# Kernel optimization log

Measured on AMD Instinct MI355X. Metric: run time of the kernel, lower is better.

The kernel has to match this reference:

```python
import jax, jax.numpy as jnp
import numpy as np

NEG_SLOPE = 0.2  # PyG GATConv default negative_slope


def gat_conv(x, edge_index, W, att_src, att_dst, bias):
    """PyG-style GATConv (concat heads, add_self_loops=True, eval mode).
    x: [N, F_in], edge_index: [2, E] (row 0 = src j, row 1 = dst i).
    W: [F_in, H*C], att_src/att_dst: [H, C], bias: [H*C].
    """
    N = x.shape[0]
    H, C = att_src.shape
    loops = jnp.arange(N, dtype=edge_index.dtype)
    src = jnp.concatenate([edge_index[0], loops])  # [E+N]
    dst = jnp.concatenate([edge_index[1], loops])
    h = (x @ W).reshape(N, H, C)                              # [N,H,C]
    a_src = jnp.einsum('nhc,hc->nh', h, att_src)              # [N,H]
    a_dst = jnp.einsum('nhc,hc->nh', h, att_dst)
    alpha = jax.nn.leaky_relu(a_src[src] + a_dst[dst], NEG_SLOPE)  # [E+N,H]
    # segment softmax over edges sharing the same destination node
    m = jax.ops.segment_max(alpha, dst, num_segments=N)       # [N,H]
    e = jnp.exp(alpha - jax.lax.stop_gradient(m)[dst])
    denom = jax.ops.segment_sum(e, dst, num_segments=N)       # [N,H]
    a = e / (denom[dst] + 1e-16)                              # [E+N,H]
    msg = h[src] * a[:, :, None]                              # [E+N,H,C]
    out = jax.ops.segment_sum(msg, dst, num_segments=N)       # [N,H,C]
    return out.reshape(N, H * C) + bias


def setup_inputs() -> dict:
    key = jax.random.key(0)
    ks = jax.random.split(key, 10)
    N, F, NC, C1, H1 = 50000, 128, 40, 16, 8
    E = 800000
    x = jax.random.normal(ks[0], (N, F), dtype=jnp.float32)
    edge_index = jax.random.randint(ks[1], (2, E), 0, N, dtype=jnp.int64)
    s1 = 1.0 / np.sqrt(F)
    W1 = jax.random.uniform(ks[2], (F, H1 * C1), jnp.float32, -s1, s1)
    att_src1 = jax.random.uniform(ks[3], (H1, C1), jnp.float32, -1.0, 1.0) * s1
    att_dst1 = jax.random.uniform(ks[4], (H1, C1), jnp.float32, -1.0, 1.0) * s1
    bias1 = jnp.zeros((H1 * C1,), jnp.float32)
    s2 = 1.0 / np.sqrt(H1 * C1)
    W2 = jax.random.uniform(ks[5], (H1 * C1, NC), jnp.float32, -s2, s2)
    att_src2 = jax.random.uniform(ks[6], (1, NC), jnp.float32, -1.0, 1.0) * s2
    att_dst2 = jax.random.uniform(ks[7], (1, NC), jnp.float32, -1.0, 1.0) * s2
    bias2 = jnp.zeros((NC,), jnp.float32)
    return {"x": x, "edge_index": edge_index, "W1": W1, "att_src1": att_src1,
            "att_dst1": att_dst1, "bias1": bias1, "W2": W2, "att_src2": att_src2,
            "att_dst2": att_dst2, "bias2": bias2}


def reference(x, edge_index, W1, att_src1, att_dst1, bias1, W2, att_src2, att_dst2, bias2):
    h = gat_conv(x, edge_index, W1, att_src1, att_dst1, bias1)   # [N, 128]
    # dropout in eval mode = identity
    out = gat_conv(h, edge_index, W2, att_src2, att_dst2, bias2)  # [N, 40]
    return out
```

## Files before the change

### kernel.cpp

```cpp
#include <hip/hip_runtime.h>
#include <hip/hip_bf16.h>
#include <math.h>

#define NEG_SLOPE 0.2f

typedef __bf16 bf16x8 __attribute__((ext_vector_type(8)));
typedef float f32x4 __attribute__((ext_vector_type(4)));

__device__ __forceinline__ float lrelu(float x) { return x > 0.f ? x : NEG_SLOPE * x; }

__device__ __forceinline__ unsigned short f2bfu(float f) {
    unsigned int ua = __float_as_uint(f);
    return (unsigned short)((ua + 0x7fffu + ((ua >> 16) & 1u)) >> 16);
}
__device__ __forceinline__ float bfu2f(unsigned short u) {
    return __uint_as_float(((unsigned int)u) << 16);
}
__device__ __forceinline__ float bf_lo(unsigned int u) { return __uint_as_float(u << 16); }
__device__ __forceinline__ float bf_hi(unsigned int u) { return __uint_as_float(u & 0xffff0000u); }

__global__ __launch_bounds__(256) void k_prep(const float* __restrict__ W1,
                                              bf16x8* __restrict__ Wp,
                                              const float* __restrict__ W2,
                                              bf16x8* __restrict__ W2p,
                                              int* __restrict__ cnt, int N) {
    int g = blockIdx.x * 256 + threadIdx.x;
    if (g < 2048) {
        int n = g & 15, quad = (g >> 4) & 3, c = (g >> 6) & 3, ct = g >> 8;
        bf16x8 v;
#pragma unroll
        for (int j = 0; j < 8; ++j)
            v[j] = (__bf16)W1[(c * 32 + quad * 8 + j) * 128 + ct * 16 + n];
        Wp[g] = v;
    } else if (g < 2816) {
        int idx = g - 2048;
        int n = idx & 15, quad = (idx >> 4) & 3, c = (idx >> 6) & 3, ct = idx >> 8;
        int colc = ct * 16 + n;
        bf16x8 v;
#pragma unroll
        for (int j = 0; j < 8; ++j)
            v[j] = (colc < 40) ? (__bf16)W2[(c * 32 + quad * 8 + j) * 40 + colc] : (__bf16)0.f;
        W2p[idx] = v;
    }
    if (g < N) cnt[g] = 0;
}

__global__ __launch_bounds__(256) void k_hist(const int* __restrict__ ei, int E, int N,
                                              int* __restrict__ cnt,
                                              unsigned short* __restrict__ rank) {
    int e = blockIdx.x * 256 + threadIdx.x;
    if (e >= E + N) return;
    int d = (e < E) ? ei[E + e] : (e - E);
    rank[e] = (unsigned short)atomicAdd(&cnt[d], 1);
}

__global__ __launch_bounds__(256) void k_scan_part(const int* __restrict__ cnt, int N,
                                                   int* __restrict__ psum) {
    __shared__ int sh[256];
    int t = threadIdx.x;
    int base = blockIdx.x * 1024 + t * 4;
    int tl = 0;
#pragma unroll
    for (int j = 0; j < 4; ++j) tl += (base + j < N) ? cnt[base + j] : 0;
    sh[t] = tl; __syncthreads();
    for (int off = 128; off > 0; off >>= 1) {
        if (t < off) sh[t] += sh[t + off];
        __syncthreads();
    }
    if (t == 0) psum[blockIdx.x] = sh[0];
}

__global__ __launch_bounds__(256) void k_scan_add(const int* __restrict__ cnt, int N,
                                                  const int* __restrict__ psum,
                                                  int* __restrict__ rowptr) {
    __shared__ int sh[256];
    __shared__ int basep;
    int t = threadIdx.x;
    if (t == 0) {
        int s = 0;
        for (int i = 0; i < blockIdx.x; ++i) s += psum[i];
        basep = s;
    }
    int base = blockIdx.x * 1024 + t * 4;
    int c[4]; int tl = 0;
#pragma unroll
    for (int j = 0; j < 4; ++j) { c[j] = (base + j < N) ? cnt[base + j] : 0; tl += c[j]; }
    sh[t] = tl; __syncthreads();
    for (int off = 1; off < 256; off <<= 1) {
        int a = (t >= off) ? sh[t - off] : 0;
        __syncthreads();
        sh[t] += a;
        __syncthreads();
    }
    int run = basep + (sh[t] - tl);
#pragma unroll
    for (int j = 0; j < 4; ++j) {
        if (base + j < N) { rowptr[base + j] = run; run += c[j]; }
    }
}

__global__ __launch_bounds__(256) void k_scatter(const int* __restrict__ ei, int E, int N,
                                                 const int* __restrict__ rowptr,
                                                 const unsigned short* __restrict__ rank,
                                                 unsigned short* __restrict__ col) {
    int e = blockIdx.x * 256 + threadIdx.x;
    if (e >= E + N) return;
    int s, d;
    if (e < E) { s = ei[e]; d = ei[E + e]; } else { s = d = e - E; }
    col[rowptr[d] + (int)rank[e]] = (unsigned short)s;
}

__global__ __launch_bounds__(256) void k_gemm1(const float* __restrict__ x,
                                               const bf16x8* __restrict__ Wp,
                                               const float* __restrict__ att_s,
                                               const float* __restrict__ att_d,
                                               unsigned short* __restrict__ h1A,
                                               unsigned short* __restrict__ h1B,
                                               float* __restrict__ a_src,
                                               float* __restrict__ a_dst, int N) {
    int t = threadIdx.x;
    int w = t >> 6, lane = t & 63, quad = lane >> 4, n16 = lane & 15;
    int row0 = blockIdx.x * 64 + w * 16;
    int arow = row0 + n16; if (arow >= N) arow = N - 1;
    const float* px = x + (size_t)arow * 128;

    bf16x8 ah[4], al[4];
#pragma unroll
    for (int c = 0; c < 4; ++c) {
        float4 v0 = *(const float4*)&px[c * 32 + quad * 8];
        float4 v1 = *(const float4*)&px[c * 32 + quad * 8 + 4];
        float xf[8] = {v0.x, v0.y, v0.z, v0.w, v1.x, v1.y, v1.z, v1.w};
#pragma unroll
        for (int j = 0; j < 8; ++j) {
            __bf16 hi = (__bf16)xf[j];
            ah[c][j] = hi;
            al[c][j] = (__bf16)(xf[j] - (float)hi);
        }
    }

    f32x4 acc[8];
#pragma unroll
    for (int ct = 0; ct < 8; ++ct) acc[ct] = (f32x4){0.f, 0.f, 0.f, 0.f};

    const uint4* wp4 = (const uint4*)Wp;
#pragma unroll
    for (int ct = 0; ct < 8; ++ct) {
#pragma unroll
        for (int c = 0; c < 4; ++c) {
            union { uint4 u; bf16x8 b; } bu;
            bu.u = wp4[((ct * 4 + c) * 4 + quad) * 16 + n16];
            acc[ct] = __builtin_amdgcn_mfma_f32_16x16x32_bf16(ah[c], bu.b, acc[ct], 0, 0, 0);
            acc[ct] = __builtin_amdgcn_mfma_f32_16x16x32_bf16(al[c], bu.b, acc[ct], 0, 0, 0);
        }
    }

    float asv[8], adv[8];
#pragma unroll
    for (int ct = 0; ct < 8; ++ct) {
        asv[ct] = att_s[ct * 16 + n16];
        adv[ct] = att_d[ct * 16 + n16];
    }
    int nodeb = row0 + quad * 4;
#pragma unroll
    for (int ct = 0; ct < 8; ++ct) {
        unsigned short* hp = (ct < 4) ? h1A : h1B;
        int chl = (ct & 3) * 16 + n16;
#pragma unroll
        for (int reg = 0; reg < 4; ++reg) {
            int node = nodeb + reg;
            float hv = acc[ct][reg];
            float ps = hv * asv[ct];
            float pd = hv * adv[ct];
#pragma unroll
            for (int m = 1; m < 16; m <<= 1) {
                ps += __shfl_xor(ps, m);
                pd += __shfl_xor(pd, m);
            }
            if (node < N) {
                hp[(size_t)node * 64 + chl] = f2bfu(hv);
                if (n16 == 0) {
                    a_src[(size_t)node * 8 + ct] = ps;
                    a_dst[(size_t)node * 8 + ct] = pd;
                }
            }
        }
    }
}

__global__ __launch_bounds__(256) void k_aggr1(const int* __restrict__ rowptr,
                                               const int* __restrict__ cnt,
                                               const unsigned short* __restrict__ col,
                                               const float* __restrict__ a_src,
                                               const float* __restrict__ a_dst,
                                               const unsigned int* __restrict__ h1A,
                                               const unsigned int* __restrict__ h1B,
                                               const float* __restrict__ bias1,
                                               unsigned int* __restrict__ out1h,
                                               unsigned int* __restrict__ out1l,
                                               int N, int nag) {
    __shared__ float evs[4][2][128];
    __shared__ int   cls[4][2][32];
    int p = (blockIdx.x >= nag) ? 1 : 0;
    int blk = blockIdx.x - p * nag;
    const uint4* hp4 = (const uint4*)(p ? h1B : h1A);
    int t = threadIdx.x;
    int w = t >> 6;
    int lane = t & 63;
    int half = lane >> 5;
    int u = lane & 31;
    int e4 = u >> 3;
    int v  = u & 7;
    int hh = v >> 1;
    int node = blk * 8 + w * 2 + half;
    bool nv = (node < N);
    int nodec = nv ? node : (N - 1);
    int beg = rowptr[nodec];
    int deg = nv ? cnt[nodec] : 0;
    int degO = __shfl_xor(deg, 32);
    int degmax = (deg > degO) ? deg : degO;
    if (degmax <= 0) return;

    float4 ad4 = *(const float4*)&a_dst[(size_t)nodec * 8 + p * 4];
    float* myev = &evs[w][half][0];
    int*   mycl = &cls[w][half][0];

    float den = 0.f;
    float nm[8];
#pragma unroll
    for (int k = 0; k < 8; ++k) nm[k] = 0.f;

    int c = 0;
    while (c < degmax) {
        int slot = c + u;
        int slotc = (slot < deg) ? slot : (deg - 1);
        if (slotc < 0) slotc = 0;
        int su = (int)col[beg + slotc];
        float4 as4 = *(const float4*)&a_src[(size_t)su * 8 + p * 4];
        bool valid = (slot < deg);
        float e0 = valid ? __expf(lrelu(as4.x + ad4.x)) : 0.f;
        float e1 = valid ? __expf(lrelu(as4.y + ad4.y)) : 0.f;
        float e2 = valid ? __expf(lrelu(as4.z + ad4.z)) : 0.f;
        float e3 = valid ? __expf(lrelu(as4.w + ad4.w)) : 0.f;
        *(float4*)&myev[u * 4] = make_float4(e0, e1, e2, e3);
        mycl[u] = su;

        int ccm = degmax - c; ccm = (ccm < 32) ? ccm : 32;
        int ng = (ccm + 3) >> 2;
        int gl = ng - 1;
        int g1 = (1 < gl) ? 1 : gl;
        int g2 = (2 < gl) ? 2 : gl;
        int g3 = (3 < gl) ? 3 : gl;
        uint4 U0 = hp4[mycl[e4] * 8 + v];
        uint4 U1 = hp4[mycl[g1 * 4 + e4] * 8 + v];
        uint4 U2 = hp4[mycl[g2 * 4 + e4] * 8 + v];
        uint4 U3 = hp4[mycl[g3 * 4 + e4] * 8 + v];
        int body = ng - 4;
        int g = 0;
#pragma unroll 2
        for (; g < body; ++g) {
            uint4 UN = hp4[mycl[(g + 4) * 4 + e4] * 8 + v];
            float ev = myev[(g * 4 + e4) * 4 + hh];
            den += ev;
            nm[0] = fmaf(ev, bf_lo(U0.x), nm[0]);
            nm[1] = fmaf(ev, bf_hi(U0.x), nm[1]);
            nm[2] = fmaf(ev, bf_lo(U0.y), nm[2]);
            nm[3] = fmaf(ev, bf_hi(U0.y), nm[3]);
            nm[4] = fmaf(ev, bf_lo(U0.z), nm[4]);
            nm[5] = fmaf(ev, bf_hi(U0.z), nm[5]);
            nm[6] = fmaf(ev, bf_lo(U0.w), nm[6]);
            nm[7] = fmaf(ev, bf_hi(U0.w), nm[7]);
            U0 = U1; U1 = U2; U2 = U3; U3 = UN;
        }
        for (; g < ng; ++g) {
            float ev = myev[(g * 4 + e4) * 4 + hh];
            den += ev;
            nm[0] = fmaf(ev, bf_lo(U0.x), nm[0]);
            nm[1] = fmaf(ev, bf_hi(U0.x), nm[1]);
            nm[2] = fmaf(ev, bf_lo(U0.y), nm[2]);
            nm[3] = fmaf(ev, bf_hi(U0.y), nm[3]);
            nm[4] = fmaf(ev, bf_lo(U0.z), nm[4]);
            nm[5] = fmaf(ev, bf_hi(U0.z), nm[5]);
            nm[6] = fmaf(ev, bf_lo(U0.w), nm[6]);
            nm[7] = fmaf(ev, bf_hi(U0.w), nm[7]);
            U0 = U1; U1 = U2; U2 = U3;
        }
        c += 32;
    }
    den += __shfl_xor(den, 8);
    den += __shfl_xor(den, 16);
#pragma unroll
    for (int k = 0; k < 8; ++k) {
        nm[k] += __shfl_xor(nm[k], 8);
        nm[k] += __shfl_xor(nm[k], 16);
    }
    if (nv && e4 == 0) {
        float inv = 1.f / (den + 1e-16f);
        float4 b0 = *(const float4*)&bias1[p * 64 + v * 8];
        float4 b1 = *(const float4*)&bias1[p * 64 + v * 8 + 4];
        float bb[8] = {b0.x, b0.y, b0.z, b0.w, b1.x, b1.y, b1.z, b1.w};
        unsigned int H[4], L[4];
#pragma unroll
        for (int q = 0; q < 4; ++q) {
            float o0 = fmaf(nm[2 * q],     inv, bb[2 * q]);
            float o1 = fmaf(nm[2 * q + 1], inv, bb[2 * q + 1]);
            unsigned short h0 = f2bfu(o0), h1 = f2bfu(o1);
            float l0 = o0 - bfu2f(h0), l1 = o1 - bfu2f(h1);
            H[q] = (unsigned int)h0 | ((unsigned int)h1 << 16);
            L[q] = (unsigned int)f2bfu(l0) | ((unsigned int)f2bfu(l1) << 16);
        }
        size_t idx = (size_t)node * 64 + p * 32 + v * 4;
        *(uint4*)&out1h[idx] = make_uint4(H[0], H[1], H[2], H[3]);
        *(uint4*)&out1l[idx] = make_uint4(L[0], L[1], L[2], L[3]);
    }
}

__global__ __launch_bounds__(256) void k_gemm2(const unsigned int* __restrict__ out1h,
                                               const unsigned int* __restrict__ out1l,
                                               const bf16x8* __restrict__ W2p,
                                               const float* __restrict__ att_s2,
                                               const float* __restrict__ att_d2,
                                               unsigned short* __restrict__ h2s,
                                               float* __restrict__ a_src2,
                                               float* __restrict__ a_dst2, int N) {
    int t = threadIdx.x;
    int w = t >> 6, lane = t & 63, quad = lane >> 4, n16 = lane & 15;
    int row0 = blockIdx.x * 64 + w * 16;
    int arow = row0 + n16; if (arow >= N) arow = N - 1;

    bf16x8 ah[4], al[4];
#pragma unroll
    for (int c = 0; c < 4; ++c) {
        size_t base = (size_t)arow * 64 + (c * 32 + quad * 8) / 2;
        union { uint4 u; bf16x8 b; } hu, lu;
        hu.u = *(const uint4*)&out1h[base];
        lu.u = *(const uint4*)&out1l[base];
        ah[c] = hu.b;
        al[c] = lu.b;
    }

    f32x4 acc[3];
#pragma unroll
    for (int ct = 0; ct < 3; ++ct) acc[ct] = (f32x4){0.f, 0.f, 0.f, 0.f};

    const uint4* wp4 = (const uint4*)W2p;
#pragma unroll
    for (int ct = 0; ct < 3; ++ct) {
#pragma unroll
        for (int c = 0; c < 4; ++c) {
            union { uint4 u; bf16x8 b; } bu;
            bu.u = wp4[((ct * 4 + c) * 4 + quad) * 16 + n16];
            acc[ct] = __builtin_amdgcn_mfma_f32_16x16x32_bf16(ah[c], bu.b, acc[ct], 0, 0, 0);
            acc[ct] = __builtin_amdgcn_mfma_f32_16x16x32_bf16(al[c], bu.b, acc[ct], 0, 0, 0);
        }
    }

    float asv[3], adv[3];
#pragma unroll
    for (int ct = 0; ct < 3; ++ct) {
        int ch = ct * 16 + n16;
        asv[ct] = (ch < 40) ? att_s2[ch] : 0.f;
        adv[ct] = (ch < 40) ? att_d2[ch] : 0.f;
    }
    int nodeb = row0 + quad * 4;
#pragma unroll
    for (int reg = 0; reg < 4; ++reg) {
        int node = nodeb + reg;
        float ps = 0.f, pd = 0.f;
#pragma unroll
        for (int ct = 0; ct < 3; ++ct) {
            float hv = acc[ct][reg];
            ps = fmaf(hv, asv[ct], ps);
            pd = fmaf(hv, adv[ct], pd);
            int ch = ct * 16 + n16;
            if (node < N && ch < 40) h2s[(size_t)node * 64 + ch] = f2bfu(hv);
        }
#pragma unroll
        for (int m = 1; m < 16; m <<= 1) {
            ps += __shfl_xor(ps, m);
            pd += __shfl_xor(pd, m);
        }
        if (node < N && n16 == 0) {
            a_src2[node] = ps;
            a_dst2[node] = pd;
        }
    }
}

__global__ __launch_bounds__(256) void k_aggr2(const int* __restrict__ rowptr,
                                               const int* __restrict__ cnt,
                                               const unsigned short* __restrict__ col,
                                               const float* __restrict__ a_src,
                                               const float* __restrict__ a_dst,
                                               const unsigned int* __restrict__ h2b,
                                               const float* __restrict__ bias2,
                                               float* __restrict__ out, int N) {
    __shared__ float evs[4][2][32];
    __shared__ int   cls[4][2][32];
    int t = threadIdx.x;
    int w = t >> 6;
    int lane = t & 63;
    int half = lane >> 5;
    int u = lane & 31;
    int e4 = u >> 3;
    int v  = u & 7;
    int node = blockIdx.x * 8 + w * 2 + half;
    bool nv = (node < N);
    int nodec = nv ? node : (N - 1);
    int beg = rowptr[nodec];
    int deg = nv ? cnt[nodec] : 0;
    int degO = __shfl_xor(deg, 32);
    int degmax = (deg > degO) ? deg : degO;
    if (degmax <= 0) return;

    const uint4* h24 = (const uint4*)h2b;
    float ad = a_dst[nodec];
    float* myev = &evs[w][half][0];
    int*   mycl = &cls[w][half][0];

    float den = 0.f;
    float am[8];
#pragma unroll
    for (int k = 0; k < 8; ++k) am[k] = 0.f;

    int c = 0;
    while (c < degmax) {
        int slot = c + u;
        int slotc = (slot < deg) ? slot : (deg - 1);
        if (slotc < 0) slotc = 0;
        int su = (int)col[beg + slotc];
        float ev = (slot < deg) ? __expf(lrelu(a_src[su] + ad)) : 0.f;
        myev[u] = ev;
        mycl[u] = su;

        int ccm = degmax - c; ccm = (ccm < 32) ? ccm : 32;
        int ng = (ccm + 3) >> 2;
        int gl = ng - 1;
        int g1 = (1 < gl) ? 1 : gl;
        int g2 = (2 < gl) ? 2 : gl;
        int g3 = (3 < gl) ? 3 : gl;
        uint4 U0 = h24[mycl[e4] * 8 + v];
        uint4 U1 = h24[mycl[g1 * 4 + e4] * 8 + v];
        uint4 U2 = h24[mycl[g2 * 4 + e4] * 8 + v];
        uint4 U3 = h24[mycl[g3 * 4 + e4] * 8 + v];
        int body = ng - 4;
        int g = 0;
#pragma unroll 2
        for (; g < body; ++g) {
            uint4 UN = h24[mycl[(g + 4) * 4 + e4] * 8 + v];
            float evv = myev[g * 4 + e4];
            den += evv;
            am[0] = fmaf(evv, bf_lo(U0.x), am[0]);
            am[1] = fmaf(evv, bf_hi(U0.x), am[1]);
            am[2] = fmaf(evv, bf_lo(U0.y), am[2]);
            am[3] = fmaf(evv, bf_hi(U0.y), am[3]);
            am[4] = fmaf(evv, bf_lo(U0.z), am[4]);
            am[5] = fmaf(evv, bf_hi(U0.z), am[5]);
            am[6] = fmaf(evv, bf_lo(U0.w), am[6]);
            am[7] = fmaf(evv, bf_hi(U0.w), am[7]);
            U0 = U1; U1 = U2; U2 = U3; U3 = UN;
        }
        for (; g < ng; ++g) {
            float evv = myev[g * 4 + e4];
            den += evv;
            am[0] = fmaf(evv, bf_lo(U0.x), am[0]);
            am[1] = fmaf(evv, bf_hi(U0.x), am[1]);
            am[2] = fmaf(evv, bf_lo(U0.y), am[2]);
            am[3] = fmaf(evv, bf_hi(U0.y), am[3]);
            am[4] = fmaf(evv, bf_lo(U0.z), am[4]);
            am[5] = fmaf(evv, bf_hi(U0.z), am[5]);
            am[6] = fmaf(evv, bf_lo(U0.w), am[6]);
            am[7] = fmaf(evv, bf_hi(U0.w), am[7]);
            U0 = U1; U1 = U2; U2 = U3;
        }
        c += 32;
    }
    den += __shfl_xor(den, 8);
    den += __shfl_xor(den, 16);
#pragma unroll
    for (int k = 0; k < 8; ++k) {
        am[k] += __shfl_xor(am[k], 8);
        am[k] += __shfl_xor(am[k], 16);
    }
    if (nv && e4 == 0 && v < 5) {
        float inv = 1.f / (den + 1e-16f);
        float4 b0 = *(const float4*)&bias2[v * 8];
        float4 b1 = *(const float4*)&bias2[v * 8 + 4];
        float4 o0 = make_float4(fmaf(am[0], inv, b0.x), fmaf(am[1], inv, b0.y),
                                fmaf(am[2], inv, b0.z), fmaf(am[3], inv, b0.w));
        float4 o1 = make_float4(fmaf(am[4], inv, b1.x), fmaf(am[5], inv, b1.y),
                                fmaf(am[6], inv, b1.z), fmaf(am[7], inv, b1.w));
        size_t ob = (size_t)node * 40 + v * 8;
        *(float4*)&out[ob] = o0;
        *(float4*)&out[ob + 4] = o1;
    }
}

extern "C" void kernel_launch(void* const* d_in, const int* in_sizes, int n_in,
                              void* d_out, int out_size, void* d_ws, size_t ws_size,
                              hipStream_t stream) {
    const float* x   = (const float*)d_in[0];
    const int*   ei  = (const int*)d_in[1];
    const float* W1  = (const float*)d_in[2];
    const float* as1 = (const float*)d_in[3];
    const float* ad1 = (const float*)d_in[4];
    const float* b1  = (const float*)d_in[5];
    const float* W2  = (const float*)d_in[6];
    const float* as2 = (const float*)d_in[7];
    const float* ad2 = (const float*)d_in[8];
    const float* b2  = (const float*)d_in[9];

    int N = in_sizes[0] / 128;
    int E = in_sizes[1] / 2;
    int EN = E + N;
    size_t Np = (size_t)((N + 3) & ~3);
    size_t ENp = ((size_t)EN + 3) & ~3;

    float* ws = (float*)d_ws;
    unsigned int* out1h = (unsigned int*)ws; ws += Np * 64;
    unsigned int* out1l = (unsigned int*)ws; ws += Np * 64;
    unsigned int* h1A = (unsigned int*)ws; ws += Np * 32;
    unsigned int* h1Bp = (unsigned int*)ws; ws += Np * 32;
    unsigned int* h2b = (unsigned int*)ws; ws += Np * 32;
    float* a_src1  = ws; ws += Np * 8;
    float* a_dst1  = ws; ws += Np * 8;
    float* a_src2v = ws; ws += Np;
    float* a_dst2v = ws; ws += Np;
    bf16x8* Wp  = (bf16x8*)ws; ws += 2048 * 4;
    bf16x8* W2p = (bf16x8*)ws; ws += 768 * 4;
    int* cnt    = (int*)ws; ws += Np;
    int* rowptr = (int*)ws; ws += Np;
    int* psum   = (int*)ws; ws += 256;
    unsigned short* col  = (unsigned short*)ws; ws += ENp / 2 + 4;
    unsigned short* rank = (unsigned short*)ws; ws += ENp / 2 + 4;

    int nb = (N + 1023) / 1024;
    int npre = (N > 2816 ? N : 2816);

    k_prep<<<(npre + 255) / 256, 256, 0, stream>>>(W1, Wp, W2, W2p, cnt, N);
    k_hist<<<(EN + 255) / 256, 256, 0, stream>>>(ei, E, N, cnt, rank);
    k_scan_part<<<nb, 256, 0, stream>>>(cnt, N, psum);
    k_scan_add<<<nb, 256, 0, stream>>>(cnt, N, psum, rowptr);
    k_scatter<<<(EN + 255) / 256, 256, 0, stream>>>(ei, E, N, rowptr, rank, col);

    k_gemm1<<<(N + 63) / 64, 256, 0, stream>>>(x, Wp, as1, ad1,
                                               (unsigned short*)h1A, (unsigned short*)h1Bp,
                                               a_src1, a_dst1, N);
    int nag = (N + 7) / 8;
    k_aggr1<<<2 * nag, 256, 0, stream>>>(rowptr, cnt, col, a_src1, a_dst1,
                                         h1A, h1Bp, b1, out1h, out1l, N, nag);
    k_gemm2<<<(N + 63) / 64, 256, 0, stream>>>(out1h, out1l, W2p, as2, ad2,
                                               (unsigned short*)h2b, a_src2v, a_dst2v, N);
    k_aggr2<<<nag, 256, 0, stream>>>(rowptr, cnt, col, a_src2v, a_dst2v, h2b, b2, (float*)d_out, N);
}
```

Before: 232.6 us.

## Precompute layer-1 edge attention exponentials in CSR scatter kernel

Moves gemm1 ahead of CSR construction so the scatter kernel can compute exp(leaky_relu(a_src+a_dst)) for every edge and store it in CSR order, split into two per-head-half buffers. The layer-1 aggregation then reads contiguous precomputed edge weights instead of gathering a_src by source index and recomputing exponentials. This removes a random gather and the exp work from the aggregation's inner loop. In exchange it adds about 32 bytes per edge of write plus read traffic and random float4 gathers of a_src/a_dst inside the scatter.

Result: slower. 261.8 us (+12.6%).

```diff
diff --git a/kernel.cpp b/kernel.cpp
--- a/kernel.cpp
+++ b/kernel.cpp
@@ -99,15 +99,30 @@
     }
 }
 
-__global__ __launch_bounds__(256) void k_scatter(const int* __restrict__ ei, int E, int N,
-                                                 const int* __restrict__ rowptr,
-                                                 const unsigned short* __restrict__ rank,
-                                                 unsigned short* __restrict__ col) {
+__global__ __launch_bounds__(256) void k_scatter_ev(const int* __restrict__ ei, int E, int N,
+                                                    const int* __restrict__ rowptr,
+                                                    const unsigned short* __restrict__ rank,
+                                                    unsigned short* __restrict__ col,
+                                                    const float* __restrict__ a_src,
+                                                    const float* __restrict__ a_dst,
+                                                    float* __restrict__ evA,
+                                                    float* __restrict__ evB) {
     int e = blockIdx.x * 256 + threadIdx.x;
     if (e >= E + N) return;
     int s, d;
     if (e < E) { s = ei[e]; d = ei[E + e]; } else { s = d = e - E; }
-    col[rowptr[d] + (int)rank[e]] = (unsigned short)s;
+    int slot = rowptr[d] + (int)rank[e];
+    col[slot] = (unsigned short)s;
+    float4 asA = *(const float4*)&a_src[(size_t)s * 8];
+    float4 asB = *(const float4*)&a_src[(size_t)s * 8 + 4];
+    float4 adA = *(const float4*)&a_dst[(size_t)d * 8];
+    float4 adB = *(const float4*)&a_dst[(size_t)d * 8 + 4];
+    float4 eA = make_float4(__expf(lrelu(asA.x + adA.x)), __expf(lrelu(asA.y + adA.y)),
+                            __expf(lrelu(asA.z + adA.z)), __expf(lrelu(asA.w + adA.w)));
+    float4 eB = make_float4(__expf(lrelu(asB.x + adB.x)), __expf(lrelu(asB.y + adB.y)),
+                            __expf(lrelu(asB.z + adB.z)), __expf(lrelu(asB.w + adB.w)));
+    *(float4*)&evA[(size_t)slot * 4] = eA;
+    *(float4*)&evB[(size_t)slot * 4] = eB;
 }
 
 __global__ __launch_bounds__(256) void k_gemm1(const float* __restrict__ x,
@@ -190,8 +205,8 @@
 __global__ __launch_bounds__(256) void k_aggr1(const int* __restrict__ rowptr,
                                                const int* __restrict__ cnt,
                                                const unsigned short* __restrict__ col,
-                                               const float* __restrict__ a_src,
-                                               const float* __restrict__ a_dst,
+                                               const float* __restrict__ evA,
+                                               const float* __restrict__ evB,
                                                const unsigned int* __restrict__ h1A,
                                                const unsigned int* __restrict__ h1B,
                                                const float* __restrict__ bias1,
@@ -203,6 +218,7 @@
     int p = (blockIdx.x >= nag) ? 1 : 0;
     int blk = blockIdx.x - p * nag;
     const uint4* hp4 = (const uint4*)(p ? h1B : h1A);
+    const float4* evp = (const float4*)(p ? evB : evA);
     int t = threadIdx.x;
     int w = t >> 6;
     int lane = t & 63;
@@ -220,7 +236,6 @@
     int degmax = (deg > degO) ? deg : degO;
     if (degmax <= 0) return;
 
-    float4 ad4 = *(const float4*)&a_dst[(size_t)nodec * 8 + p * 4];
     float* myev = &evs[w][half][0];
     int*   mycl = &cls[w][half][0];
 
@@ -235,13 +250,9 @@
         int slotc = (slot < deg) ? slot : (deg - 1);
         if (slotc < 0) slotc = 0;
         int su = (int)col[beg + slotc];
-        float4 as4 = *(const float4*)&a_src[(size_t)su * 8 + p * 4];
-        bool valid = (slot < deg);
-        float e0 = valid ? __expf(lrelu(as4.x + ad4.x)) : 0.f;
-        float e1 = valid ? __expf(lrelu(as4.y + ad4.y)) : 0.f;
-        float e2 = valid ? __expf(lrelu(as4.z + ad4.z)) : 0.f;
-        float e3 = valid ? __expf(lrelu(as4.w + ad4.w)) : 0.f;
-        *(float4*)&myev[u * 4] = make_float4(e0, e1, e2, e3);
+        float4 e4v = evp[beg + slotc];
+        if (slot >= deg) e4v = make_float4(0.f, 0.f, 0.f, 0.f);
+        *(float4*)&myev[u * 4] = e4v;
         mycl[u] = su;
 
         int ccm = degmax - c; ccm = (ccm < 32) ? ccm : 32;
@@ -525,6 +536,8 @@
     float* a_dst1  = ws; ws += Np * 8;
     float* a_src2v = ws; ws += Np;
     float* a_dst2v = ws; ws += Np;
+    float* evA = ws; ws += ENp * 4;
+    float* evB = ws; ws += ENp * 4;
     bf16x8* Wp  = (bf16x8*)ws; ws += 2048 * 4;
     bf16x8* W2p = (bf16x8*)ws; ws += 768 * 4;
     int* cnt    = (int*)ws; ws += Np;
@@ -537,16 +550,17 @@
     int npre = (N > 2816 ? N : 2816);
 
     k_prep<<<(npre + 255) / 256, 256, 0, stream>>>(W1, Wp, W2, W2p, cnt, N);
+    k_gemm1<<<(N + 63) / 64, 256, 0, stream>>>(x, Wp, as1, ad1,
+                                               (unsigned short*)h1A, (unsigned short*)h1Bp,
+                                               a_src1, a_dst1, N);
     k_hist<<<(EN + 255) / 256, 256, 0, stream>>>(ei, E, N, cnt, rank);
     k_scan_part<<<nb, 256, 0, stream>>>(cnt, N, psum);
     k_scan_add<<<nb, 256, 0, stream>>>(cnt, N, psum, rowptr);
-    k_scatter<<<(EN + 255) / 256, 256, 0, stream>>>(ei, E, N, rowptr, rank, col);
-
-    k_gemm1<<<(N + 63) / 64, 256, 0, stream>>>(x, Wp, as1, ad1,
-                                               (unsigned short*)h1A, (unsigned short*)h1Bp,
-                                               a_src1, a_dst1, N);
+    k_scatter_ev<<<(EN + 255) / 256, 256, 0, stream>>>(ei, E, N, rowptr, rank, col,
+                                                       a_src1, a_dst1, evA, evB);
+
     int nag = (N + 7) / 8;
-    k_aggr1<<<2 * nag, 256, 0, stream>>>(rowptr, cnt, col, a_src1, a_dst1,
+    k_aggr1<<<2 * nag, 256, 0, stream>>>(rowptr, cnt, col, evA, evB,
                                          h1A, h1Bp, b1, out1h, out1l, N, nag);
     k_gemm2<<<(N + 63) / 64, 256, 0, stream>>>(out1h, out1l, W2p, as2, ad2,
                                                (unsigned short*)h2b, a_src2v, a_dst2v, N);
```
